# Kernel tuning notes

Hardware: AMD Instinct MI355X
Metric: run time of the kernel (lower is better)

## Reference

```python
import jax, jax.numpy as jnp
import numpy as np

B, N, R, VR = 4, 10475, 48, 96


def setup_inputs() -> dict:
    key = jax.random.key(0)
    k1, k2, k3, k4 = jax.random.split(key, 4)
    v1s = jax.random.normal(k1, (B, N, 3), dtype=jnp.float32)
    v2s = jax.random.normal(k2, (B, N, 3), dtype=jnp.float32)
    cmaps = jax.random.randint(k3, (B, R, R), 0, 2).astype(bool)
    rid_to_vid = jax.random.randint(k4, (R, VR), 0, N, dtype=jnp.int32)
    return {"v1s": v1s, "v2s": v2s, "cmaps": cmaps, "rid_to_vid": rid_to_vid}


def reference(v1s, v2s, cmaps, rid_to_vid):
    # Gather region vertex subsets for ALL regions at once: [B, R, Vr, 3]
    g1 = v1s[:, rid_to_vid, :]
    g2 = v2s[:, rid_to_vid, :]
    # Squared norms per point
    sq1 = jnp.sum(g1 * g1, axis=-1)                 # [B, R, Vr]
    sq2 = jnp.sum(g2 * g2, axis=-1)                 # [B, R, Vr]
    # Inner products for every (region r of person1, region s of person2) pair
    inner = jnp.einsum('brvc,bswc->brsvw', g1, g2)  # [B, R, R, Vr, Vr]
    d2 = sq1[:, :, None, :, None] + sq2[:, None, :, None, :] - 2.0 * inner
    d = jnp.sqrt(jnp.maximum(d2, 0.0))              # squared=False -> euclidean
    # min over the two vertex-subset axes -> per region-pair min distance [B, R, R]
    min_d = jnp.min(d, axis=(3, 4))
    # Original averages min dists only over active contact pairs (torch.where(cmap))
    m = cmaps.astype(min_d.dtype)                   # [B, R, R]
    return jnp.sum(min_d * m, axis=(1, 2)) / jnp.sum(m, axis=(1, 2))
```

## Files before the change

kernel.cpp:

```cpp
#include <hip/hip_runtime.h>

#define B_ 4
#define R_ 48
#define VR_ 96
#define NBLK_CELL (B_ * R_ * 12)

typedef float v2f __attribute__((ext_vector_type(2)));

__device__ __forceinline__ int detect_stride4(const unsigned char* cm, int t) {
  const unsigned int d = ((const unsigned int*)cm)[t];
  const unsigned int b1 = (d >> 8) & 0xff, b2 = (d >> 16) & 0xff, b3 = d >> 24;
  const unsigned long long nzm = __ballot((b1 | b2 | b3) != 0);
  const unsigned long long bigm = __ballot((b1 > 1) || (b2 > 1) || (b3 > 1));
  return (bigm != 0ull || nzm == 0ull) ? 1 : 0;
}

__global__ __launch_bounds__(256) void fused_cell_kernel(
    const float* __restrict__ v1s, const float* __restrict__ v2s,
    const int* __restrict__ rid_to_vid, const unsigned char* __restrict__ cm,
    float* __restrict__ minbuf, int N) {
  const int bid = blockIdx.x;
  const int b = bid / (R_ * 12);
  const int rem = bid % (R_ * 12);
  const int r = rem / 12;
  const int quad = rem % 12;
  const int t = threadIdx.x;
  const int w = t >> 6, lane = t & 63;
  const int s = quad * 4 + w;
  const int cellIdx = (b * R_ + r) * R_ + s;

  __shared__ int stride4_s;
  if (t < 64) {
    const int s4 = detect_stride4(cm, t);
    if (t == 0) stride4_s = s4;
  }
  __syncthreads();
  const int stride4 = stride4_s;

  const bool active = stride4 ? (((const unsigned int*)cm)[cellIdx] != 0u)
                              : (cm[cellIdx] != 0);

  __shared__ int flags[4];
  if (lane == 0) flags[w] = active ? 1 : 0;
  __syncthreads();
  if ((flags[0] | flags[1] | flags[2] | flags[3]) == 0) return;

  __shared__ float s1[3 * VR_];
  __shared__ float s2[4][3 * VR_];
  if (t < VR_) {
    const int idx = rid_to_vid[r * VR_ + t];
    const float* src = v1s + ((size_t)b * N + idx) * 3;
    s1[t] = src[0]; s1[VR_ + t] = src[1]; s1[2 * VR_ + t] = src[2];
  }
  for (int p = t; p < 4 * VR_; p += 256) {
    const int srow = p / VR_, v = p % VR_;
    const int idx = rid_to_vid[(quad * 4 + srow) * VR_ + v];
    const float* src = v2s + ((size_t)b * N + idx) * 3;
    s2[srow][v] = src[0]; s2[srow][VR_ + v] = src[1]; s2[srow][2 * VR_ + v] = src[2];
  }
  __syncthreads();
  if (!active) return;

  const float* r2 = s2[w];
  const int hi = lane >> 3, lo = lane & 7;

  float Ax[12], Ay[12], Az[12];
  v2f Bx[6], By[6], Bz[6];
#pragma unroll
  for (int k = 0; k < 3; ++k) {
    *(float4*)&Ax[4 * k] = *(const float4*)(s1            + hi * 12 + 4 * k);
    *(float4*)&Ay[4 * k] = *(const float4*)(s1 +     VR_  + hi * 12 + 4 * k);
    *(float4*)&Az[4 * k] = *(const float4*)(s1 + 2 * VR_  + hi * 12 + 4 * k);
    *(float4*)&Bx[2 * k] = *(const float4*)(r2            + lo * 12 + 4 * k);
    *(float4*)&By[2 * k] = *(const float4*)(r2 +     VR_  + lo * 12 + 4 * k);
    *(float4*)&Bz[2 * k] = *(const float4*)(r2 + 2 * VR_  + lo * 12 + 4 * k);
  }

  float acc[4] = {3.4e38f, 3.4e38f, 3.4e38f, 3.4e38f};
#pragma unroll
  for (int i = 0; i < 12; ++i) {
    const v2f axx = {Ax[i], Ax[i]};
    const v2f ayy = {Ay[i], Ay[i]};
    const v2f azz = {Az[i], Az[i]};
#pragma unroll
    for (int j = 0; j < 6; ++j) {
      const v2f dx = axx - Bx[j];
      const v2f dy = ayy - By[j];
      const v2f dz = azz - Bz[j];
      const v2f d2 = dx * dx + dy * dy + dz * dz;
      acc[j & 3] = fminf(acc[j & 3], fminf(d2.x, d2.y));
    }
  }
  float mind2 = fminf(fminf(acc[0], acc[1]), fminf(acc[2], acc[3]));
#pragma unroll
  for (int off = 32; off > 0; off >>= 1)
    mind2 = fminf(mind2, __shfl_down(mind2, off, 64));
  if (lane == 0) minbuf[cellIdx] = sqrtf(fmaxf(mind2, 0.0f));
}

__global__ __launch_bounds__(256) void finalize_kernel(
    const float* __restrict__ min_d, const unsigned char* __restrict__ cm,
    float* __restrict__ out) {
  const int b = blockIdx.x;
  const int t = threadIdx.x;

  __shared__ int stride4_s;
  if (t < 64) {
    const int s4 = detect_stride4(cm, t);
    if (t == 0) stride4_s = s4;
  }
  __syncthreads();
  const int stride4 = stride4_s;
  const unsigned int* cm32 = (const unsigned int*)cm;

  float sum = 0.0f, cnt = 0.0f;
  for (int i = t; i < R_ * R_; i += 256) {
    const int gi = b * R_ * R_ + i;
    const bool m = stride4 ? (cm32[gi] != 0u) : (cm[gi] != 0);
    if (m) { sum += min_d[gi]; cnt += 1.0f; }
  }
#pragma unroll
  for (int off = 32; off > 0; off >>= 1) {
    sum += __shfl_down(sum, off, 64);
    cnt += __shfl_down(cnt, off, 64);
  }
  __shared__ float ws_[4], wc_[4];
  if ((t & 63) == 0) { ws_[t >> 6] = sum; wc_[t >> 6] = cnt; }
  __syncthreads();
  if (t == 0) {
    out[b] = (ws_[0] + ws_[1] + ws_[2] + ws_[3]) /
             (wc_[0] + wc_[1] + wc_[2] + wc_[3]);
  }
}

extern "C" void kernel_launch(void* const* d_in, const int* in_sizes, int n_in,
                              void* d_out, int out_size, void* d_ws, size_t ws_size,
                              hipStream_t stream) {
  const float* v1s = (const float*)d_in[0];
  const float* v2s = (const float*)d_in[1];
  const unsigned char* cmaps = (const unsigned char*)d_in[2];
  const int* rid_to_vid = (const int*)d_in[3];
  float* out = (float*)d_out;
  float* minbuf = (float*)d_ws;

  const int N = in_sizes[0] / (B_ * 3);

  fused_cell_kernel<<<NBLK_CELL, 256, 0, stream>>>(
      v1s, v2s, rid_to_vid, cmaps, minbuf, N);
  finalize_kernel<<<B_, 256, 0, stream>>>(minbuf, cmaps, out);
}
```

Baseline: 23.26 us.

## Fuse finalize reduction into cell kernel via per-block atomic accumulation

Removes the separate finalize kernel. Each block now recounts the active cells for its batch, divides its partial sum of min distances by that count, and atomically adds the result into the output, which a memset zeroes first. This trades one kernel launch for a memset plus redundant per-block mask counting (2304 mask reads per block) and float atomics, which make the summation order nondeterministic.

```diff
diff --git a/kernel.cpp b/kernel.cpp
--- a/kernel.cpp
+++ b/kernel.cpp
@@ -3,7 +3,7 @@
 #define B_ 4
 #define R_ 48
 #define VR_ 96
-#define NBLK_CELL (B_ * R_ * 12)
+#define NBLK (B_ * R_ * 12)
 
 typedef float v2f __attribute__((ext_vector_type(2)));
 
@@ -15,10 +15,10 @@
   return (bigm != 0ull || nzm == 0ull) ? 1 : 0;
 }
 
-__global__ __launch_bounds__(256) void fused_cell_kernel(
+__global__ __launch_bounds__(256) void fused_all_kernel(
     const float* __restrict__ v1s, const float* __restrict__ v2s,
     const int* __restrict__ rid_to_vid, const unsigned char* __restrict__ cm,
-    float* __restrict__ minbuf, int N) {
+    float* __restrict__ out, int N) {
   const int bid = blockIdx.x;
   const int b = bid / (R_ * 12);
   const int rem = bid % (R_ * 12);
@@ -36,14 +36,23 @@
   }
   __syncthreads();
   const int stride4 = stride4_s;
+  const unsigned int* cm32 = (const unsigned int*)cm;
 
-  const bool active = stride4 ? (((const unsigned int*)cm)[cellIdx] != 0u)
-                              : (cm[cellIdx] != 0);
+  const bool active = stride4 ? (cm32[cellIdx] != 0u) : (cm[cellIdx] != 0);
 
   __shared__ int flags[4];
   if (lane == 0) flags[w] = active ? 1 : 0;
   __syncthreads();
   if ((flags[0] | flags[1] | flags[2] | flags[3]) == 0) return;
+
+  int cnt = 0;
+  const int base = b * R_ * R_;
+  for (int i = t; i < R_ * R_; i += 256)
+    cnt += stride4 ? (cm32[base + i] != 0u ? 1 : 0) : (cm[base + i] != 0 ? 1 : 0);
+#pragma unroll
+  for (int off = 32; off > 0; off >>= 1) cnt += __shfl_down(cnt, off, 64);
+  __shared__ int wcnt[4];
+  if (lane == 0) wcnt[w] = cnt;
 
   __shared__ float s1[3 * VR_];
   __shared__ float s2[4][3 * VR_];
@@ -59,77 +68,53 @@
     s2[srow][v] = src[0]; s2[srow][VR_ + v] = src[1]; s2[srow][2 * VR_ + v] = src[2];
   }
   __syncthreads();
-  if (!active) return;
 
-  const float* r2 = s2[w];
-  const int hi = lane >> 3, lo = lane & 7;
+  float mind = 0.0f;
+  if (active) {
+    const float* r2 = s2[w];
+    const int hi = lane >> 3, lo = lane & 7;
 
-  float Ax[12], Ay[12], Az[12];
-  v2f Bx[6], By[6], Bz[6];
+    float Ax[12], Ay[12], Az[12];
+    v2f Bx[6], By[6], Bz[6];
 #pragma unroll
-  for (int k = 0; k < 3; ++k) {
-    *(float4*)&Ax[4 * k] = *(const float4*)(s1            + hi * 12 + 4 * k);
-    *(float4*)&Ay[4 * k] = *(const float4*)(s1 +     VR_  + hi * 12 + 4 * k);
-    *(float4*)&Az[4 * k] = *(const float4*)(s1 + 2 * VR_  + hi * 12 + 4 * k);
-    *(float4*)&Bx[2 * k] = *(const float4*)(r2            + lo * 12 + 4 * k);
-    *(float4*)&By[2 * k] = *(const float4*)(r2 +     VR_  + lo * 12 + 4 * k);
-    *(float4*)&Bz[2 * k] = *(const float4*)(r2 + 2 * VR_  + lo * 12 + 4 * k);
+    for (int k = 0; k < 3; ++k) {
+      *(float4*)&Ax[4 * k] = *(const float4*)(s1           + hi * 12 + 4 * k);
+      *(float4*)&Ay[4 * k] = *(const float4*)(s1 +     VR_ + hi * 12 + 4 * k);
+      *(float4*)&Az[4 * k] = *(const float4*)(s1 + 2 * VR_ + hi * 12 + 4 * k);
+      *(float4*)&Bx[2 * k] = *(const float4*)(r2           + lo * 12 + 4 * k);
+      *(float4*)&By[2 * k] = *(const float4*)(r2 +     VR_ + lo * 12 + 4 * k);
+      *(float4*)&Bz[2 * k] = *(const float4*)(r2 + 2 * VR_ + lo * 12 + 4 * k);
+    }
+
+    float acc[4] = {3.4e38f, 3.4e38f, 3.4e38f, 3.4e38f};
+#pragma unroll
+    for (int i = 0; i < 12; ++i) {
+      const v2f axx = {Ax[i], Ax[i]};
+      const v2f ayy = {Ay[i], Ay[i]};
+      const v2f azz = {Az[i], Az[i]};
+#pragma unroll
+      for (int j = 0; j < 6; ++j) {
+        const v2f dx = axx - Bx[j];
+        const v2f dy = ayy - By[j];
+        const v2f dz = azz - Bz[j];
+        const v2f d2 = dx * dx + dy * dy + dz * dz;
+        acc[j & 3] = fminf(acc[j & 3], fminf(d2.x, d2.y));
+      }
+    }
+    float mind2 = fminf(fminf(acc[0], acc[1]), fminf(acc[2], acc[3]));
+#pragma unroll
+    for (int off = 32; off > 0; off >>= 1)
+      mind2 = fminf(mind2, __shfl_down(mind2, off, 64));
+    mind = sqrtf(fmaxf(mind2, 0.0f));
   }
 
-  float acc[4] = {3.4e38f, 3.4e38f, 3.4e38f, 3.4e38f};
-#pragma unroll
-  for (int i = 0; i < 12; ++i) {
-    const v2f axx = {Ax[i], Ax[i]};
-    const v2f ayy = {Ay[i], Ay[i]};
-    const v2f azz = {Az[i], Az[i]};
-#pragma unroll
-    for (int j = 0; j < 6; ++j) {
-      const v2f dx = axx - Bx[j];
-      const v2f dy = ayy - By[j];
-      const v2f dz = azz - Bz[j];
-      const v2f d2 = dx * dx + dy * dy + dz * dz;
-      acc[j & 3] = fminf(acc[j & 3], fminf(d2.x, d2.y));
-    }
-  }
-  float mind2 = fminf(fminf(acc[0], acc[1]), fminf(acc[2], acc[3]));
-#pragma unroll
-  for (int off = 32; off > 0; off >>= 1)
-    mind2 = fminf(mind2, __shfl_down(mind2, off, 64));
-  if (lane == 0) minbuf[cellIdx] = sqrtf(fmaxf(mind2, 0.0f));
-}
-
-__global__ __launch_bounds__(256) void finalize_kernel(
-    const float* __restrict__ min_d, const unsigned char* __restrict__ cm,
-    float* __restrict__ out) {
-  const int b = blockIdx.x;
-  const int t = threadIdx.x;
-
-  __shared__ int stride4_s;
-  if (t < 64) {
-    const int s4 = detect_stride4(cm, t);
-    if (t == 0) stride4_s = s4;
-  }
-  __syncthreads();
-  const int stride4 = stride4_s;
-  const unsigned int* cm32 = (const unsigned int*)cm;
-
-  float sum = 0.0f, cnt = 0.0f;
-  for (int i = t; i < R_ * R_; i += 256) {
-    const int gi = b * R_ * R_ + i;
-    const bool m = stride4 ? (cm32[gi] != 0u) : (cm[gi] != 0);
-    if (m) { sum += min_d[gi]; cnt += 1.0f; }
-  }
-#pragma unroll
-  for (int off = 32; off > 0; off >>= 1) {
-    sum += __shfl_down(sum, off, 64);
-    cnt += __shfl_down(cnt, off, 64);
-  }
-  __shared__ float ws_[4], wc_[4];
-  if ((t & 63) == 0) { ws_[t >> 6] = sum; wc_[t >> 6] = cnt; }
+  __shared__ float sm[4];
+  if (lane == 0) sm[w] = mind;
   __syncthreads();
   if (t == 0) {
-    out[b] = (ws_[0] + ws_[1] + ws_[2] + ws_[3]) /
-             (wc_[0] + wc_[1] + wc_[2] + wc_[3]);
+    const float count_b = (float)(wcnt[0] + wcnt[1] + wcnt[2] + wcnt[3]);
+    const float partial = (sm[0] + sm[1] + sm[2] + sm[3]) / count_b;
+    atomicAdd(&out[b], partial);
   }
 }
 
@@ -141,11 +126,10 @@
   const unsigned char* cmaps = (const unsigned char*)d_in[2];
   const int* rid_to_vid = (const int*)d_in[3];
   float* out = (float*)d_out;
-  float* minbuf = (float*)d_ws;
 
   const int N = in_sizes[0] / (B_ * 3);
 
-  fused_cell_kernel<<<NBLK_CELL, 256, 0, stream>>>(
-      v1s, v2s, rid_to_vid, cmaps, minbuf, N);
-  finalize_kernel<<<B_, 256, 0, stream>>>(minbuf, cmaps, out);
+  hipMemsetAsync(out, 0, (size_t)out_size * sizeof(float), stream);
+  fused_all_kernel<<<NBLK, 256, 0, stream>>>(
+      v1s, v2s, rid_to_vid, cmaps, out, N);
 }
```

Measured after the change: 45.77 us. +96.7%, slower.

## Tile cells as 4x4 region blocks so each block reuses gathered rows

Applied to the files above, without the earlier changes.

Each block now covers a 4x4 tile of (r, s) region pairs instead of 1x4, so gathered vertex data for both persons is loaded once into shared memory and reused across 16 cells. Each wave loops over four s-regions and skips inactive cells with a per-wave mask. The gather now runs before the activity check and the early-exit barrier is gone. Grid size drops from 2304 to 576 blocks, which reduces redundant global gathers but lowers parallelism and puts more serial work in each wave.

```diff
diff --git a/kernel.cpp b/kernel.cpp
--- a/kernel.cpp
+++ b/kernel.cpp
@@ -3,9 +3,10 @@
 #define B_ 4
 #define R_ 48
 #define VR_ 96
-#define NBLK_CELL (B_ * R_ * 12)
+#define NBLK (B_ * 12 * 12)
 
 typedef float v2f __attribute__((ext_vector_type(2)));
+struct F3 { float x, y, z; };
 
 __device__ __forceinline__ int detect_stride4(const unsigned char* cm, int t) {
   const unsigned int d = ((const unsigned int*)cm)[t];
@@ -20,82 +21,89 @@
     const int* __restrict__ rid_to_vid, const unsigned char* __restrict__ cm,
     float* __restrict__ minbuf, int N) {
   const int bid = blockIdx.x;
-  const int b = bid / (R_ * 12);
-  const int rem = bid % (R_ * 12);
-  const int r = rem / 12;
-  const int quad = rem % 12;
+  const int b = bid / 144;
+  const int rem = bid % 144;
+  const int rq = rem / 12;
+  const int sq = rem % 12;
   const int t = threadIdx.x;
   const int w = t >> 6, lane = t & 63;
-  const int s = quad * 4 + w;
-  const int cellIdx = (b * R_ + r) * R_ + s;
 
   __shared__ int stride4_s;
   if (t < 64) {
     const int s4 = detect_stride4(cm, t);
     if (t == 0) stride4_s = s4;
   }
+
+  __shared__ float s1[4][3 * VR_];
+  __shared__ float s2[4][3 * VR_];
+#pragma unroll
+  for (int i = 0; i < 3; ++i) {
+    const int p = t + 256 * i;
+    const int row8 = p / VR_, v = p % VR_;
+    const int g2row = row8 >= 4;
+    const int rrow = g2row ? (sq * 4 + row8 - 4) : (rq * 4 + row8);
+    const int idx = rid_to_vid[rrow * VR_ + v];
+    const F3 pt = *(const F3*)((g2row ? v2s : v1s) + ((size_t)b * N + idx) * 3);
+    float* dst = g2row ? s2[row8 - 4] : s1[row8];
+    dst[v] = pt.x; dst[VR_ + v] = pt.y; dst[2 * VR_ + v] = pt.z;
+  }
   __syncthreads();
   const int stride4 = stride4_s;
+  const unsigned int* cm32 = (const unsigned int*)cm;
 
-  const bool active = stride4 ? (((const unsigned int*)cm)[cellIdx] != 0u)
-                              : (cm[cellIdx] != 0);
+  const int r = rq * 4 + w;
+  const int cellBase = (b * R_ + r) * R_ + sq * 4;
+  int actmask = 0;
+#pragma unroll
+  for (int k = 0; k < 4; ++k) {
+    const bool a = stride4 ? (cm32[cellBase + k] != 0u) : (cm[cellBase + k] != 0);
+    actmask |= a ? (1 << k) : 0;
+  }
+  if (!actmask) return;
 
-  __shared__ int flags[4];
-  if (lane == 0) flags[w] = active ? 1 : 0;
-  __syncthreads();
-  if ((flags[0] | flags[1] | flags[2] | flags[3]) == 0) return;
-
-  __shared__ float s1[3 * VR_];
-  __shared__ float s2[4][3 * VR_];
-  if (t < VR_) {
-    const int idx = rid_to_vid[r * VR_ + t];
-    const float* src = v1s + ((size_t)b * N + idx) * 3;
-    s1[t] = src[0]; s1[VR_ + t] = src[1]; s1[2 * VR_ + t] = src[2];
-  }
-  for (int p = t; p < 4 * VR_; p += 256) {
-    const int srow = p / VR_, v = p % VR_;
-    const int idx = rid_to_vid[(quad * 4 + srow) * VR_ + v];
-    const float* src = v2s + ((size_t)b * N + idx) * 3;
-    s2[srow][v] = src[0]; s2[srow][VR_ + v] = src[1]; s2[srow][2 * VR_ + v] = src[2];
-  }
-  __syncthreads();
-  if (!active) return;
-
-  const float* r2 = s2[w];
   const int hi = lane >> 3, lo = lane & 7;
+  const float* r1 = s1[w];
 
   float Ax[12], Ay[12], Az[12];
-  v2f Bx[6], By[6], Bz[6];
 #pragma unroll
   for (int k = 0; k < 3; ++k) {
-    *(float4*)&Ax[4 * k] = *(const float4*)(s1            + hi * 12 + 4 * k);
-    *(float4*)&Ay[4 * k] = *(const float4*)(s1 +     VR_  + hi * 12 + 4 * k);
-    *(float4*)&Az[4 * k] = *(const float4*)(s1 + 2 * VR_  + hi * 12 + 4 * k);
-    *(float4*)&Bx[2 * k] = *(const float4*)(r2            + lo * 12 + 4 * k);
-    *(float4*)&By[2 * k] = *(const float4*)(r2 +     VR_  + lo * 12 + 4 * k);
-    *(float4*)&Bz[2 * k] = *(const float4*)(r2 + 2 * VR_  + lo * 12 + 4 * k);
+    *(float4*)&Ax[4 * k] = *(const float4*)(r1           + hi * 12 + 4 * k);
+    *(float4*)&Ay[4 * k] = *(const float4*)(r1 +     VR_ + hi * 12 + 4 * k);
+    *(float4*)&Az[4 * k] = *(const float4*)(r1 + 2 * VR_ + hi * 12 + 4 * k);
   }
 
-  float acc[4] = {3.4e38f, 3.4e38f, 3.4e38f, 3.4e38f};
 #pragma unroll
-  for (int i = 0; i < 12; ++i) {
-    const v2f axx = {Ax[i], Ax[i]};
-    const v2f ayy = {Ay[i], Ay[i]};
-    const v2f azz = {Az[i], Az[i]};
+  for (int c = 0; c < 4; ++c) {
+    if (!(actmask & (1 << c))) continue;
+    const float* r2 = s2[c];
+    v2f Bx[6], By[6], Bz[6];
 #pragma unroll
-    for (int j = 0; j < 6; ++j) {
-      const v2f dx = axx - Bx[j];
-      const v2f dy = ayy - By[j];
-      const v2f dz = azz - Bz[j];
-      const v2f d2 = dx * dx + dy * dy + dz * dz;
-      acc[j & 3] = fminf(acc[j & 3], fminf(d2.x, d2.y));
+    for (int k = 0; k < 3; ++k) {
+      *(float4*)&Bx[2 * k] = *(const float4*)(r2           + lo * 12 + 4 * k);
+      *(float4*)&By[2 * k] = *(const float4*)(r2 +     VR_ + lo * 12 + 4 * k);
+      *(float4*)&Bz[2 * k] = *(const float4*)(r2 + 2 * VR_ + lo * 12 + 4 * k);
     }
+    float acc[4] = {3.4e38f, 3.4e38f, 3.4e38f, 3.4e38f};
+#pragma unroll
+    for (int i = 0; i < 12; ++i) {
+      const v2f axx = {Ax[i], Ax[i]};
+      const v2f ayy = {Ay[i], Ay[i]};
+      const v2f azz = {Az[i], Az[i]};
+#pragma unroll
+      for (int j = 0; j < 6; ++j) {
+        const v2f dx = axx - Bx[j];
+        const v2f dy = ayy - By[j];
+        const v2f dz = azz - Bz[j];
+        const v2f d2 = dx * dx + dy * dy + dz * dz;
+        acc[j & 3] = fminf(acc[j & 3], fminf(d2.x, d2.y));
+      }
+    }
+    float mind2 = fminf(fminf(acc[0], acc[1]), fminf(acc[2], acc[3]));
+#pragma unroll
+    for (int off = 32; off > 0; off >>= 1)
+      mind2 = fminf(mind2, __shfl_down(mind2, off, 64));
+    if (lane == 0) minbuf[cellBase + c] = sqrtf(fmaxf(mind2, 0.0f));
   }
-  float mind2 = fminf(fminf(acc[0], acc[1]), fminf(acc[2], acc[3]));
-#pragma unroll
-  for (int off = 32; off > 0; off >>= 1)
-    mind2 = fminf(mind2, __shfl_down(mind2, off, 64));
-  if (lane == 0) minbuf[cellIdx] = sqrtf(fmaxf(mind2, 0.0f));
 }
 
 __global__ __launch_bounds__(256) void finalize_kernel(
@@ -145,7 +153,7 @@
 
   const int N = in_sizes[0] / (B_ * 3);
 
-  fused_cell_kernel<<<NBLK_CELL, 256, 0, stream>>>(
+  fused_cell_kernel<<<NBLK, 256, 0, stream>>>(
       v1s, v2s, rid_to_vid, cmaps, minbuf, N);
   finalize_kernel<<<B_, 256, 0, stream>>>(minbuf, cmaps, out);
 }
```

New measurement: 26.54 us. 1.14x slower.
